# Optimization experiments

Measured on AMD Instinct MI355X. Metric: run time of the kernel, lower is better.

Reference implementation:

```python
import jax, jax.numpy as jnp
import numpy as np

T, N, E = 12, 2048, 32768
X_DIM, H_DIM, Z_DIM, NL = 128, 256, 32, 2
EPS = 1e-10


def setup_inputs() -> dict:
    key = jax.random.key(0)
    ks = jax.random.split(key, 24)
    s = 0.1  # reset_parameters stdv
    p = {}
    p['x'] = jax.random.normal(ks[0], (T, N, X_DIM), jnp.float32)
    p['edge_index'] = jax.random.randint(ks[1], (T, 2, E), 0, N, dtype=jnp.int32)
    p['adj'] = (jax.random.uniform(ks[2], (T, N, N)) < 0.01).astype(jnp.float32)
    p['eps_src'] = jax.random.normal(ks[3], (T, N, Z_DIM), jnp.float32)
    p['eps_dst'] = jax.random.normal(ks[4], (T, N, Z_DIM), jnp.float32)
    p['phi_x_w'] = s * jax.random.normal(ks[5], (X_DIM, H_DIM), jnp.float32)
    p['phi_z_w'] = s * jax.random.normal(ks[6], (2 * Z_DIM, H_DIM), jnp.float32)
    p['gru_xw0'] = s * jax.random.normal(ks[7], (3, 2 * H_DIM, H_DIM), jnp.float32)  # (z,r,h) layer 0
    p['gru_xw1'] = s * jax.random.normal(ks[8], (3, H_DIM, H_DIM), jnp.float32)      # (z,r,h) layer 1
    p['gru_hw'] = s * jax.random.normal(ks[9], (NL, 3, H_DIM, H_DIM), jnp.float32)
    p['enc_w'] = s * jax.random.normal(ks[10], (2, 2 * H_DIM, H_DIM), jnp.float32)   # [src,dst]
    p['enc_b'] = s * jax.random.normal(ks[11], (2, H_DIM), jnp.float32)
    p['mean_w'] = s * jax.random.normal(ks[12], (2, H_DIM, Z_DIM), jnp.float32)
    p['mean_b'] = s * jax.random.normal(ks[13], (2, Z_DIM), jnp.float32)
    p['std_w'] = s * jax.random.normal(ks[14], (2, H_DIM, Z_DIM), jnp.float32)
    p['std_b'] = s * jax.random.normal(ks[15], (2, Z_DIM), jnp.float32)
    p['pri_w'] = s * jax.random.normal(ks[16], (2, H_DIM, H_DIM), jnp.float32)
    p['pri_b'] = s * jax.random.normal(ks[17], (2, H_DIM), jnp.float32)
    p['pri_mw'] = s * jax.random.normal(ks[18], (2, H_DIM, Z_DIM), jnp.float32)
    p['pri_mb'] = s * jax.random.normal(ks[19], (2, Z_DIM), jnp.float32)
    p['pri_sw'] = s * jax.random.normal(ks[20], (2, H_DIM, Z_DIM), jnp.float32)
    p['pri_sb'] = s * jax.random.normal(ks[21], (2, Z_DIM), jnp.float32)
    return p


def _gin_pre(x, src, dst):
    # GIN (eps=0): x + sum_{(src->dst)} x[src]; linear applied by caller
    return x + jax.ops.segment_sum(x[src], dst, num_segments=N)


def _gcn(x, w, b, src, dst):
    # GCNConv with self-loops and symmetric normalization
    deg = jax.ops.segment_sum(jnp.ones(src.shape[0], x.dtype), dst, num_segments=N) + 1.0
    dinv = deg ** -0.5
    nrm = dinv[src] * dinv[dst]
    xw = x @ w
    agg = jax.ops.segment_sum(nrm[:, None] * xw[src], dst, num_segments=N)
    return agg + xw / deg[:, None] + b


def _kld(m1, s1, m2, s2):
    k = (2 * jnp.log(s2 + EPS) - 2 * jnp.log(s1 + EPS)
         + ((s1 + EPS) ** 2 + (m1 - m2) ** 2) / (s2 + EPS) ** 2 - 1.0)
    return 0.5 / N * jnp.mean(jnp.sum(k, axis=1))


def reference(x, edge_index, adj, eps_src, eps_dst, phi_x_w, phi_z_w,
              gru_xw0, gru_xw1, gru_hw, enc_w, enc_b, mean_w, mean_b,
              std_w, std_b, pri_w, pri_b, pri_mw, pri_mb, pri_sw, pri_sb):
    h0 = jnp.zeros((NL, N, H_DIM), x.dtype)

    def step(h, inp):
        x_t, e_t, a_t, es_t, ed_t = inp
        src, dst = e_t[0], e_t[1]
        phi_x_t = jax.nn.relu(x_t @ phi_x_w)
        cat = jnp.concatenate([phi_x_t, h[-1]], axis=1)  # [N, 2H]
        cat_pre = _gin_pre(cat, src, dst)
        enc_s = jax.nn.relu(cat_pre @ enc_w[0] + enc_b[0])
        enc_d = jax.nn.relu(cat_pre @ enc_w[1] + enc_b[1])
        mean_s = _gcn(enc_s, mean_w[0], mean_b[0], src, dst)
        std_s = jax.nn.softplus(_gin_pre(enc_s, src, dst) @ std_w[0] + std_b[0])
        mean_d = _gcn(enc_d, mean_w[1], mean_b[1], src, dst)
        std_d = jax.nn.softplus(_gin_pre(enc_d, src, dst) @ std_w[1] + std_b[1])
        pri_s = jax.nn.relu(h[-1] @ pri_w[0] + pri_b[0])
        pm_s = pri_s @ pri_mw[0] + pri_mb[0]
        ps_s = jax.nn.softplus(pri_s @ pri_sw[0] + pri_sb[0])
        pri_d = jax.nn.relu(h[-1] @ pri_w[1] + pri_b[1])
        pm_d = pri_d @ pri_mw[1] + pri_mb[1]
        ps_d = jax.nn.softplus(pri_d @ pri_sw[1] + pri_sb[1])
        z_s = mean_s + std_s * es_t
        z_d = mean_d + std_d * ed_t
        phi_z_t = jax.nn.relu(jnp.concatenate([z_s, z_d], axis=1) @ phi_z_w)
        dec = z_s @ z_d.T  # [N, N] inner-product decoder (identity act)
        # graph-GRU across layers
        g_in = jnp.concatenate([phi_x_t, phi_z_t], axis=1)  # [N, 2H]
        new_h = []
        for i in range(NL):
            xi = g_in if i == 0 else new_h[i - 1]
            xw = gru_xw0 if i == 0 else gru_xw1
            xpre = _gin_pre(xi, src, dst)
            hpre = _gin_pre(h[i], src, dst)
            z_g = jax.nn.sigmoid(xpre @ xw[0] + hpre @ gru_hw[i, 0])
            r_g = jax.nn.sigmoid(xpre @ xw[1] + hpre @ gru_hw[i, 1])
            h_t = jnp.tanh(xpre @ xw[2] + _gin_pre(r_g * h[i], src, dst) @ gru_hw[i, 2])
            new_h.append(z_g * h[i] + (1.0 - z_g) * h_t)
        h_new = jnp.stack(new_h)
        kld = _kld(mean_s, std_s, pm_s, ps_s) + _kld(mean_d, std_d, pm_d, ps_d)
        ssum = a_t.sum()
        nn2 = jnp.asarray(N * N, a_t.dtype)
        posw = (nn2 - ssum) / ssum
        norm = nn2 / ((nn2 - ssum) * 2.0)
        bce = -posw * a_t * jax.nn.log_sigmoid(dec) - (1.0 - a_t) * jax.nn.log_sigmoid(-dec)
        nll = norm * jnp.mean(bce)
        return h_new, (kld, nll, dec)

    _, (klds, nlls, decs) = jax.lax.scan(step, h0, (x, edge_index, adj, eps_src, eps_dst))
    return jnp.sum(klds), jnp.sum(nlls), decs
```

## Files before the change

### kernel.cpp

```cpp
#include <hip/hip_runtime.h>
#include <math.h>

#define NTS 12
#define NND 2048
#define NED 32768
#define XDI 128
#define HDI 256
#define ZDI 32
#define EPSC 1e-10f
#define NH ((size_t)NND * HDI)
#define NZ ((size_t)NND * ZDI)
#define ZPL ((size_t)NND * 64)
#define XSZ ((size_t)NTS * NND * XDI)

typedef unsigned short u16;
typedef __bf16 bf16x8 __attribute__((ext_vector_type(8)));
typedef float f32x4 __attribute__((ext_vector_type(4)));

#define MF(a, b, c) __builtin_amdgcn_mfma_f32_16x16x32_bf16(a, b, c, 0, 0, 0)


__device__ __forceinline__ float lsigf(float x) {
    return fminf(x, 0.f) - log1pf(expf(-fabsf(x)));
}
__device__ __forceinline__ float splus(float v) {
    return fmaxf(v, 0.f) + log1pf(expf(-fabsf(v)));
}
__device__ __forceinline__ u16 f2b(float f) {
    unsigned u = __float_as_uint(f);
    u += 0x7fffu + ((u >> 16) & 1u);
    return (u16)(u >> 16);
}
__device__ __forceinline__ float b2f(u16 b) {
    return __uint_as_float((unsigned)b << 16);
}
__device__ __forceinline__ void f2b2(float v, u16& hi, u16& lo) {
    hi = f2b(v);
    lo = f2b(v - b2f(hi));
}
__device__ __forceinline__ void st_b16(u16* buf, size_t plane, size_t idx, float v) {
    u16 hi, lo;
    f2b2(v, hi, lo);
    buf[idx] = hi;
    buf[plane + idx] = lo;
}
__device__ __forceinline__ void st_b16v4(u16* buf, size_t plane, size_t idx, float4 v) {
    ushort4 h, l;
    f2b2(v.x, h.x, l.x); f2b2(v.y, h.y, l.y);
    f2b2(v.z, h.z, l.z); f2b2(v.w, h.w, l.w);
    *(ushort4*)(buf + idx) = h;
    *(ushort4*)(buf + plane + idx) = l;
}
__device__ __forceinline__ float4 ld_hl4(const u16* b, size_t plane, size_t idx) {
    ushort4 h = *(const ushort4*)(b + idx);
    ushort4 l = *(const ushort4*)(b + plane + idx);
    float4 r;
    r.x = b2f(h.x) + b2f(l.x); r.y = b2f(h.y) + b2f(l.y);
    r.z = b2f(h.z) + b2f(l.z); r.w = b2f(h.w) + b2f(l.w);
    return r;
}
__device__ float4 gin_hl(const u16* buf, size_t plane, int n, const int* __restrict__ offs,
                         const int* __restrict__ cs, int lane) {
    int e0 = offs[n], e1 = offs[n + 1];
    size_t c4 = (size_t)lane * 4;
    float4 a0 = ld_hl4(buf, plane, (size_t)n * HDI + c4);
    float4 a1 = {0.f, 0.f, 0.f, 0.f}, a2 = {0.f, 0.f, 0.f, 0.f}, a3 = {0.f, 0.f, 0.f, 0.f};
    int j = e0;
    for (; j + 3 < e1; j += 4) {
        int s0 = cs[j], s1 = cs[j + 1], s2 = cs[j + 2], s3 = cs[j + 3];
        float4 v0 = ld_hl4(buf, plane, (size_t)s0 * HDI + c4);
        float4 v1 = ld_hl4(buf, plane, (size_t)s1 * HDI + c4);
        float4 v2 = ld_hl4(buf, plane, (size_t)s2 * HDI + c4);
        float4 v3 = ld_hl4(buf, plane, (size_t)s3 * HDI + c4);
        a0.x += v0.x; a0.y += v0.y; a0.z += v0.z; a0.w += v0.w;
        a1.x += v1.x; a1.y += v1.y; a1.z += v1.z; a1.w += v1.w;
        a2.x += v2.x; a2.y += v2.y; a2.z += v2.z; a2.w += v2.w;
        a3.x += v3.x; a3.y += v3.y; a3.z += v3.z; a3.w += v3.w;
    }
    for (; j < e1; ++j) {
        float4 v = ld_hl4(buf, plane, (size_t)cs[j] * HDI + c4);
        a0.x += v.x; a0.y += v.y; a0.z += v.z; a0.w += v.w;
    }
    a0.x += a1.x + a2.x + a3.x;
    a0.y += a1.y + a2.y + a3.y;
    a0.z += a1.z + a2.z + a3.z;
    a0.w += a1.w + a2.w + a3.w;
    return a0;
}

__host__ __device__ inline size_t wtoff(int m) {
    if (m == 0) return 0;
    if (m == 1) return 65536;
    return 98304 + (size_t)(m - 2) * 131072;
}

__device__ __forceinline__ void mm64(f32x4* A12, const u16* __restrict__ Ahi, size_t apl,
                                     const u16* __restrict__ Bt, int K,
                                     int row0, int cc, int lr, int kg) {
    const u16* bp = Bt + (size_t)(cc * 16 + lr) * K + kg;
    const u16* blp = bp + (size_t)K * HDI;
    const u16* ap0 = Ahi + (size_t)(row0 + lr) * K + kg;
    for (int k0 = 0; k0 < K; k0 += 32) {
        bf16x8 bh = *(const bf16x8*)(bp + k0);
        bf16x8 bl = *(const bf16x8*)(blp + k0);
#pragma unroll
        for (int s = 0; s < 4; s++) {
            const u16* ap = ap0 + (size_t)(16 * s) * K;
            bf16x8 ah = *(const bf16x8*)(ap + k0);
            bf16x8 al = *(const bf16x8*)(ap + apl + k0);
            A12[s * 3 + 0] = MF(ah, bh, A12[s * 3 + 0]);
            A12[s * 3 + 1] = MF(al, bh, A12[s * 3 + 1]);
            A12[s * 3 + 2] = MF(ah, bl, A12[s * 3 + 2]);
        }
    }
}

__device__ __forceinline__ void epi_hl(f32x4* A12, u16* dst, size_t plane,
                                       int row0, int cc, int lane, int relu) {
    int col = cc * 16 + (lane & 15);
    int rb0 = (lane >> 4) << 2;
#pragma unroll
    for (int s = 0; s < 4; s++)
#pragma unroll
        for (int i = 0; i < 4; i++) {
            int row = row0 + s * 16 + rb0 + i;
            float v = A12[s * 3][i] + A12[s * 3 + 1][i] + A12[s * 3 + 2][i];
            if (relu) v = fmaxf(v, 0.f);
            st_b16(dst, plane, (size_t)row * HDI + col, v);
        }
}


__global__ __launch_bounds__(256) void k0_setup(const int* __restrict__ ei,
                                                const float* __restrict__ x,
                                                const float* w_phix, const float* w_phiz,
                                                const float* w_enc, const float* w_pri,
                                                const float* w_gx0, const float* w_gx1,
                                                const float* w_gh,
                                                u16* __restrict__ warena, u16* __restrict__ xb,
                                                int* __restrict__ counts) {
    const int bid = blockIdx.x, tid = threadIdx.x;
    if (bid < 1536) {
        int idx = bid * 256 + tid;
        int t = idx >> 15, e = idx & (NED - 1);
        atomicAdd(&counts[t * NND + ei[(size_t)t * 2 * NED + NED + e]], 1);
    } else if (bid < 7424) {
        int u = bid - 1536;
        int m = u >> 8, k = u & 255;
        const int Kt = (m == 0) ? 128 : (m == 1) ? 64 : 256;
        if (k < Kt) {
            const int srcsel[23] = {0, 1, 2, 2, 2, 2, 3, 3, 4, 4, 4, 4,
                                    4, 4, 6, 6, 6, 5, 5, 5, 6, 6, 6};
            const int srcoff[23] = {0, 0, 0, 65536, 131072, 196608, 0, 65536,
                                    0, 65536, 131072, 196608, 262144, 327680,
                                    0, 65536, 131072, 0, 65536, 131072,
                                    196608, 262144, 327680};
            const float* srcs[7] = {w_phix, w_phiz, w_enc, w_pri, w_gx0, w_gx1, w_gh};
            const float* W = srcs[srcsel[m]] + srcoff[m];
            u16* D = warena + wtoff(m);
            float v = W[(size_t)k * 256 + tid];
            u16 hi, lo;
            f2b2(v, hi, lo);
            D[(size_t)tid * Kt + k] = hi;
            D[(size_t)Kt * 256 + (size_t)tid * Kt + k] = lo;
        }
    } else {
        size_t i = (size_t)(bid - 7424) * 256 + tid;
        float4 v = ((const float4*)x)[i];
        ushort4 h, l;
        f2b2(v.x, h.x, l.x); f2b2(v.y, h.y, l.y);
        f2b2(v.z, h.z, l.z); f2b2(v.w, h.w, l.w);
        ((ushort4*)xb)[i] = h;
        ((ushort4*)(xb + XSZ))[i] = l;
    }
}

__global__ __launch_bounds__(256) void k1_scan_phix(const int* __restrict__ counts,
                                                    int* __restrict__ offs,
                                                    float* __restrict__ deg,
                                                    float* __restrict__ dinv,
                                                    const u16* __restrict__ xb,
                                                    const u16* __restrict__ warena,
                                                    u16* __restrict__ phixb) {
    __shared__ int tsum[256];
    const int bid = blockIdx.x, tid = threadIdx.x;
    if (bid < 12) {
        const int* cnt = counts + bid * NND;
        int* off = offs + bid * (NND + 1);
        float* dg = deg + bid * NND;
        float* dv = dinv + bid * NND;
        int base = tid * 8;
        int local[8];
        int s = 0;
        for (int i = 0; i < 8; i++) { local[i] = s; s += cnt[base + i]; }
        tsum[tid] = s;
        __syncthreads();
        for (int o = 1; o < 256; o <<= 1) {
            int v = (tid >= o) ? tsum[tid - o] : 0;
            __syncthreads();
            tsum[tid] += v;
            __syncthreads();
        }
        int excl = tsum[tid] - s;
        for (int i = 0; i < 8; i++) off[base + i] = excl + local[i];
        if (tid == 255) off[NND] = excl + s;
        for (int i = 0; i < 8; i++) {
            float d = (float)cnt[base + i] + 1.0f;
            dg[base + i] = d;
            dv[base + i] = 1.0f / sqrtf(d);
        }
    } else {
        int u = bid - 12;
        int t = u >> 7, tile = u & 127;
        const int wid = tid >> 6, lane = tid & 63;
        const int lr = lane & 15, kg = (lane >> 4) * 8;
        int row0 = (tile >> 4) * 256 + wid * 64, cc = tile & 15;
        f32x4 A12[12] = {};
        mm64(A12, xb + (size_t)t * NND * XDI, XSZ, warena + wtoff(0), XDI, row0, cc, lr, kg);
        epi_hl(A12, phixb + (size_t)t * 2 * NH, NH, row0, cc, lane, 1);
    }
}

__global__ __launch_bounds__(256) void k2_fill(const int* __restrict__ ei,
                                               const int* __restrict__ offs,
                                               int* __restrict__ cursor,
                                               const float* __restrict__ dinv,
                                               int* __restrict__ csrc,
                                               float* __restrict__ csrw) {
    int idx = blockIdx.x * 256 + threadIdx.x;
    int t = idx >> 15, e = idx & (NED - 1);
    const int* src = ei + (size_t)t * 2 * NED;
    const int* dst = src + NED;
    int d = dst[e], s = src[e];
    const int* off_t = offs + t * (NND + 1);
    int pos = off_t[d] + atomicAdd(&cursor[t * NND + d], 1);
    csrc[(size_t)t * NED + pos] = s;
    csrw[(size_t)t * NED + pos] = dinv[t * NND + s] * dinv[t * NND + d];
}


__global__ __launch_bounds__(256) void kA(const u16* __restrict__ phxt,
                                          const u16* __restrict__ h1b,
                                          const u16* __restrict__ warena,
                                          u16* __restrict__ Ub, float* __restrict__ prif,
                                          const float* __restrict__ b_pri) {
    const int bid = blockIdx.x, tid = threadIdx.x;
    const int wid = tid >> 6, lane = tid & 63;
    const int lr = lane & 15, kg = (lane >> 4) * 8;
    f32x4 A12[12] = {};
    if (bid < 256) {
        int o = bid >> 7, tile = bid & 127;
        int row0 = (tile >> 4) * 256 + wid * 64, cc = tile & 15;
        mm64(A12, phxt, NH, warena + wtoff(2 + 2 * o), HDI, row0, cc, lr, kg);
        mm64(A12, h1b, NH, warena + wtoff(3 + 2 * o), HDI, row0, cc, lr, kg);
        epi_hl(A12, Ub + (size_t)o * 2 * NH, NH, row0, cc, lane, 0);
    } else {
        int q = bid - 256;
        int o = q >> 7, tile = q & 127;
        int row0 = (tile >> 4) * 256 + wid * 64, cc = tile & 15;
        mm64(A12, h1b, NH, warena + wtoff(6 + o), HDI, row0, cc, lr, kg);
        int col = cc * 16 + lr;
        int rb0 = (lane >> 4) << 2;
        float* C = prif + (size_t)o * NH;
        float bv = b_pri[o * HDI + col];
#pragma unroll
        for (int s = 0; s < 4; s++)
#pragma unroll
            for (int i = 0; i < 4; i++) {
                int row = row0 + s * 16 + rb0 + i;
                float v = A12[s * 3][i] + A12[s * 3 + 1][i] + A12[s * 3 + 2][i] + bv;
                C[(size_t)row * HDI + col] = fmaxf(v, 0.f);
            }
    }
}

__global__ __launch_bounds__(256) void kB(const u16* __restrict__ Ub,
                                          const float* __restrict__ prif,
                                          const int* __restrict__ offs,
                                          const int* __restrict__ cs,
                                          const float* __restrict__ b_enc,
                                          const float* __restrict__ w_mean,
                                          const float* __restrict__ w_std,
                                          const float* __restrict__ w_pm,
                                          const float* __restrict__ b_pm,
                                          const float* __restrict__ w_ps,
                                          const float* __restrict__ b_ps,
                                          float* __restrict__ xw, float* __restrict__ pmps) {
    __shared__ float rowbuf[4][256];
    const int tid = threadIdx.x;
    const int wid = tid >> 6, lane = tid & 63;
    const int u = blockIdx.x * 4 + wid;
    if (u < 4096) {
        int seg = u >> 11, n = u & 2047;
        float4 a = gin_hl(Ub + (size_t)seg * 2 * NH, NH, n, offs, cs, lane);
        const float* eb = b_enc + seg * HDI + lane * 4;
        a.x = fmaxf(a.x + eb[0], 0.f);
        a.y = fmaxf(a.y + eb[1], 0.f);
        a.z = fmaxf(a.z + eb[2], 0.f);
        a.w = fmaxf(a.w + eb[3], 0.f);
        *(float4*)&rowbuf[wid][lane * 4] = a;
        const float* B = ((lane < 32) ? w_mean : w_std) + seg * 8192;
        int m = lane & 31;
        float acc = 0.f;
        const float* rb = rowbuf[wid];
#pragma unroll 8
        for (int k = 0; k < 256; k++) acc += rb[k] * B[k * 32 + m];
        float* O = xw + ((lane < 32) ? seg : 2 + seg) * NZ;
        O[(size_t)n * ZDI + m] = acc;
    } else {
        int q = u - 4096;
        int s = q >> 10, unit = q & 1023;
        int n = unit * 2 + (lane >> 5);
        int m = lane & 31;
        const float* A = prif + ((s < 2) ? 0 : NH);
        const float* B = (s & 1) ? (w_ps + (s >> 1) * 8192) : (w_pm + (s >> 1) * 8192);
        const float* bi = (s & 1) ? (b_ps + (s >> 1) * 32) : (b_pm + (s >> 1) * 32);
        float acc = bi[m];
        const float* ar = A + (size_t)n * HDI;
#pragma unroll 4
        for (int k = 0; k < 256; k += 4) {
            float4 a4 = *(const float4*)(ar + k);
            acc += a4.x * B[(k + 0) * 32 + m];
            acc += a4.y * B[(k + 1) * 32 + m];
            acc += a4.z * B[(k + 2) * 32 + m];
            acc += a4.w * B[(k + 3) * 32 + m];
        }
        if (s & 1) acc = splus(acc);
        pmps[(size_t)s * NZ + (size_t)n * ZDI + m] = acc;
    }
}

__global__ __launch_bounds__(256) void kC(const float* __restrict__ xw,
                                          const float* __restrict__ pmps,
                                          const int* __restrict__ offs,
                                          const int* __restrict__ cs,
                                          const float* __restrict__ cw,
                                          const float* __restrict__ dgv,
                                          const float* __restrict__ b_mean,
                                          const float* __restrict__ b_std,
                                          const float* __restrict__ es,
                                          const float* __restrict__ ed,
                                          float* __restrict__ zcatf, u16* __restrict__ zcatb,
                                          double* __restrict__ accd) {
    __shared__ double smd[4];
    const int tid = threadIdx.x;
    const int wid = tid >> 6, lane = tid & 63;
    const int n = blockIdx.x * 4 + wid;
    const int sel = lane >> 5, m = lane & 31;
    const float* xwm = xw + (size_t)sel * NZ;
    const float* xws = xw + (size_t)(2 + sel) * NZ;
    int e0 = offs[n], e1 = offs[n + 1];
    float am0 = 0.f, am1 = 0.f, am2 = 0.f, am3 = 0.f;
    float as0 = xws[(size_t)n * ZDI + m], as1 = 0.f, as2 = 0.f, as3 = 0.f;
    int j = e0;
    for (; j + 3 < e1; j += 4) {
        int s0 = cs[j], s1 = cs[j + 1], s2 = cs[j + 2], s3 = cs[j + 3];
        am0 += cw[j] * xwm[(size_t)s0 * ZDI + m];
        am1 += cw[j + 1] * xwm[(size_t)s1 * ZDI + m];
        am2 += cw[j + 2] * xwm[(size_t)s2 * ZDI + m];
        am3 += cw[j + 3] * xwm[(size_t)s3 * ZDI + m];
        as0 += xws[(size_t)s0 * ZDI + m];
        as1 += xws[(size_t)s1 * ZDI + m];
        as2 += xws[(size_t)s2 * ZDI + m];
        as3 += xws[(size_t)s3 * ZDI + m];
    }
    for (; j < e1; ++j) {
        int s = cs[j];
        am0 += cw[j] * xwm[(size_t)s * ZDI + m];
        as0 += xws[(size_t)s * ZDI + m];
    }
    float am = am0 + am1 + am2 + am3;
    float as_ = as0 + as1 + as2 + as3;
    float mean = am + xwm[(size_t)n * ZDI + m] / dgv[n] + b_mean[sel * 32 + m];
    float sd = splus(as_ + b_std[sel * 32 + m]);
    const float* eps = sel ? ed : es;
    float z = mean + sd * eps[(size_t)n * ZDI + m];
    size_t zi = (size_t)n * 64 + sel * 32 + m;
    zcatf[zi] = z;
    st_b16(zcatb, ZPL, zi, z);
    float pm = pmps[(size_t)(sel * 2) * NZ + (size_t)n * ZDI + m];
    float ps = pmps[(size_t)(sel * 2 + 1) * NZ + (size_t)n * ZDI + m];
    float a1v = sd + EPSC, a2v = ps + EPSC;
    float dm = mean - pm;
    double kl = (double)(2.f * (logf(a2v) - logf(a1v)) +
                         (a1v * a1v + dm * dm) / (a2v * a2v) - 1.f);
#pragma unroll
    for (int o = 32; o > 0; o >>= 1) kl += __shfl_down(kl, o);
    if (lane == 0) smd[wid] = kl;
    __syncthreads();
    if (tid == 0) atomicAdd(accd, smd[0] + smd[1] + smd[2] + smd[3]);
}

__global__ __launch_bounds__(256) void kD(const float* __restrict__ zcatf,
                                          const u16* __restrict__ zcatb,
                                          const float* __restrict__ adjt,
                                          const u16* __restrict__ warena,
                                          float* __restrict__ dect,
                                          u16* __restrict__ phizb,
                                          double* __restrict__ bcet) {
    __shared__ float smf[2 * 32 * 68];
    const int bid = blockIdx.x, tid = threadIdx.x;
    if (bid < 1024) {
        float (*zsS)[68] = (float(*)[68])smf;
        float (*zdS)[68] = (float(*)[68])(smf + 32 * 68);
        const int tx = tid & 15, ty = tid >> 4;
        const int c0 = (bid & 31) * 64, r0 = (bid >> 5) * 64;
        const int lrow = tid >> 2;
        const int lk = (tid & 3) * 8;
        float4 v0 = *(const float4*)&zcatf[(size_t)(r0 + lrow) * 64 + lk];
        float4 v1 = *(const float4*)&zcatf[(size_t)(r0 + lrow) * 64 + lk + 4];
        float4 w0 = *(const float4*)&zcatf[(size_t)(c0 + lrow) * 64 + 32 + lk];
        float4 w1 = *(const float4*)&zcatf[(size_t)(c0 + lrow) * 64 + 32 + lk + 4];
        zsS[lk + 0][lrow] = v0.x; zsS[lk + 1][lrow] = v0.y; zsS[lk + 2][lrow] = v0.z; zsS[lk + 3][lrow] = v0.w;
        zsS[lk + 4][lrow] = v1.x; zsS[lk + 5][lrow] = v1.y; zsS[lk + 6][lrow] = v1.z; zsS[lk + 7][lrow] = v1.w;
        zdS[lk + 0][lrow] = w0.x; zdS[lk + 1][lrow] = w0.y; zdS[lk + 2][lrow] = w0.z; zdS[lk + 3][lrow] = w0.w;
        zdS[lk + 4][lrow] = w1.x; zdS[lk + 5][lrow] = w1.y; zdS[lk + 6][lrow] = w1.z; zdS[lk + 7][lrow] = w1.w;
        __syncthreads();

        float acc[4][4] = {};
#pragma unroll
        for (int k = 0; k < 32; k++) {
            const float4 a4 = *(const float4*)&zsS[k][ty * 4];
            const float4 b4 = *(const float4*)&zdS[k][tx * 4];
            const float aa[4] = {a4.x, a4.y, a4.z, a4.w};
            const float bb[4] = {b4.x, b4.y, b4.z, b4.w};
#pragma unroll
            for (int i = 0; i < 4; i++)
#pragma unroll
                for (int j = 0; j < 4; j++) acc[i][j] += aa[i] * bb[j];
        }

        float pa = 0.f, p1 = 0.f, p2 = 0.f;
#pragma unroll
        for (int i = 0; i < 4; i++) {
            const int r = r0 + ty * 4 + i;
            const float4 av4 = *(const float4*)&adjt[(size_t)r * NND + c0 + tx * 4];
            const float av[4] = {av4.x, av4.y, av4.z, av4.w};
            float* drow = &dect[(size_t)r * NND + c0 + tx * 4];
#pragma unroll
            for (int j = 0; j < 4; j++) {
                float d = acc[i][j];
                __builtin_nontemporal_store(d, &drow[j]);
                float a = av[j];
                pa += a;
                p1 += a * lsigf(d);
                p2 += (1.f - a) * lsigf(-d);
            }
        }
        __syncthreads();
        smf[tid] = pa; smf[256 + tid] = p1; smf[512 + tid] = p2;
        __syncthreads();
        for (int o = 128; o > 0; o >>= 1) {
            if (tid < o) {
                smf[tid] += smf[tid + o];
                smf[256 + tid] += smf[256 + tid + o];
                smf[512 + tid] += smf[512 + tid + o];
            }
            __syncthreads();
        }
        if (tid == 0) {
            double* b = bcet + (size_t)bid * 3;
            b[0] = (double)smf[0];
            b[1] = (double)smf[256];
            b[2] = (double)smf[512];
        }
    } else {
        int u = bid - 1024;
        const int wid = tid >> 6, lane = tid & 63;
        const int lr = lane & 15, kg = (lane >> 4) * 8;
        int row0 = (u >> 4) * 256 + wid * 64, cc = u & 15;
        f32x4 A12[12] = {};
        mm64(A12, zcatb, ZPL, warena + wtoff(1), 64, row0, cc, lr, kg);
        epi_hl(A12, phizb, NH, row0, cc, lane, 1);
    }
}

__global__ __launch_bounds__(256) void kE(const u16* __restrict__ phxt,
                                          const u16* __restrict__ phizb,
                                          const u16* __restrict__ h0b,
                                          const u16* __restrict__ warena,
                                          u16* __restrict__ Pb) {
    const int bid = blockIdx.x, tid = threadIdx.x;
    const int wid = tid >> 6, lane = tid & 63;
    const int lr = lane & 15, kg = (lane >> 4) * 8;
    int o = bid >> 7, tile = bid & 127;
    int row0 = (tile >> 4) * 256 + wid * 64, cc = tile & 15;
    f32x4 A12[12] = {};
    if (o == 0) {
        mm64(A12, phxt, NH, warena + wtoff(8), HDI, row0, cc, lr, kg);
        mm64(A12, phizb, NH, warena + wtoff(9), HDI, row0, cc, lr, kg);
        mm64(A12, h0b, NH, warena + wtoff(14), HDI, row0, cc, lr, kg);
    } else if (o == 1) {
        mm64(A12, phxt, NH, warena + wtoff(10), HDI, row0, cc, lr, kg);
        mm64(A12, phizb, NH, warena + wtoff(11), HDI, row0, cc, lr, kg);
        mm64(A12, h0b, NH, warena + wtoff(15), HDI, row0, cc, lr, kg);
    } else {
        mm64(A12, phxt, NH, warena + wtoff(12), HDI, row0, cc, lr, kg);
        mm64(A12, phizb, NH, warena + wtoff(13), HDI, row0, cc, lr, kg);
    }
    epi_hl(A12, Pb + (size_t)o * 2 * NH, NH, row0, cc, lane, 0);
}

__global__ __launch_bounds__(256) void kE1(const u16* __restrict__ nh0b,
                                           const u16* __restrict__ h1b,
                                           const u16* __restrict__ warena,
                                           u16* __restrict__ Pb) {
    const int bid = blockIdx.x, tid = threadIdx.x;
    const int wid = tid >> 6, lane = tid & 63;
    const int lr = lane & 15, kg = (lane >> 4) * 8;
    int o = bid >> 7, tile = bid & 127;
    int row0 = (tile >> 4) * 256 + wid * 64, cc = tile & 15;
    f32x4 A12[12] = {};
    if (o == 0) {
        mm64(A12, nh0b, NH, warena + wtoff(17), HDI, row0, cc, lr, kg);
        mm64(A12, h1b, NH, warena + wtoff(20), HDI, row0, cc, lr, kg);
    } else if (o == 1) {
        mm64(A12, nh0b, NH, warena + wtoff(18), HDI, row0, cc, lr, kg);
        mm64(A12, h1b, NH, warena + wtoff(21), HDI, row0, cc, lr, kg);
    } else {
        mm64(A12, nh0b, NH, warena + wtoff(19), HDI, row0, cc, lr, kg);
    }
    epi_hl(A12, Pb + (size_t)o * 2 * NH, NH, row0, cc, lane, 0);
}

__global__ __launch_bounds__(256) void kF(const u16* __restrict__ Pb,
                                          const u16* __restrict__ hb,
                                          float* __restrict__ zGf, u16* __restrict__ rhb,
                                          const int* __restrict__ offs,
                                          const int* __restrict__ cs) {
    const int tid = threadIdx.x;
    const int wid = tid >> 6, lane = tid & 63;
    const int u = blockIdx.x * 4 + wid;
    int seg = u >> 11, n = u & 2047;
    size_t idx = (size_t)n * HDI + lane * 4;
    if (seg == 0) {
        float4 a = gin_hl(Pb, NH, n, offs, cs, lane);
        a.x = 1.f / (1.f + expf(-a.x)); a.y = 1.f / (1.f + expf(-a.y));
        a.z = 1.f / (1.f + expf(-a.z)); a.w = 1.f / (1.f + expf(-a.w));
        *(float4*)&zGf[idx] = a;
    } else {
        float4 a = gin_hl(Pb + 2 * NH, NH, n, offs, cs, lane);
        float4 h4 = ld_hl4(hb, NH, idx);
        float4 rh;
        rh.x = h4.x / (1.f + expf(-a.x)); rh.y = h4.y / (1.f + expf(-a.y));
        rh.z = h4.z / (1.f + expf(-a.z)); rh.w = h4.w / (1.f + expf(-a.w));
        st_b16v4(rhb, NH, idx, rh);
    }
}

__global__ __launch_bounds__(256) void kG(const u16* __restrict__ rhb,
                                          const u16* __restrict__ warena, int wtm,
                                          const u16* __restrict__ Pb, u16* __restrict__ Rb) {
    const int bid = blockIdx.x, tid = threadIdx.x;
    const int wid = tid >> 6, lane = tid & 63;
    const int lr = lane & 15, kg = (lane >> 4) * 8;
    int row0 = (bid >> 4) * 256 + wid * 64, cc = bid & 15;
    f32x4 A12[12] = {};
    mm64(A12, rhb, NH, warena + wtoff(wtm), HDI, row0, cc, lr, kg);
    const u16* Ph = Pb + 4 * NH;
    int col = cc * 16 + lr;
    int rb0 = (lane >> 4) << 2;
#pragma unroll
    for (int s = 0; s < 4; s++)
#pragma unroll
        for (int i = 0; i < 4; i++) {
            int row = row0 + s * 16 + rb0 + i;
            size_t idx = (size_t)row * HDI + col;
            float v = A12[s * 3][i] + A12[s * 3 + 1][i] + A12[s * 3 + 2][i] +
                      b2f(Ph[idx]) + b2f(Ph[NH + idx]);
            st_b16(Rb, NH, idx, v);
        }
}

__global__ __launch_bounds__(256) void kH(const u16* __restrict__ Rb,
                                          const float* __restrict__ zGf,
                                          const u16* __restrict__ hb,
                                          u16* __restrict__ nhb,
                                          const int* __restrict__ offs,
                                          const int* __restrict__ cs) {
    const int tid = threadIdx.x;
    const int wid = tid >> 6, lane = tid & 63;
    const int n = blockIdx.x * 4 + wid;
    size_t idx = (size_t)n * HDI + lane * 4;
    float4 a = gin_hl(Rb, NH, n, offs, cs, lane);
    float4 z4 = *(const float4*)&zGf[idx];
    float4 h4 = ld_hl4(hb, NH, idx);
    float4 o;
    o.x = z4.x * h4.x + (1.f - z4.x) * tanhf(a.x);
    o.y = z4.y * h4.y + (1.f - z4.y) * tanhf(a.y);
    o.z = z4.z * h4.z + (1.f - z4.z) * tanhf(a.z);
    o.w = z4.w * h4.w + (1.f - z4.w) * tanhf(a.w);
    st_b16v4(nhb, NH, idx, o);
}

__global__ __launch_bounds__(256) void kFin(const double* __restrict__ accd,
                                            const double* __restrict__ bce,
                                            float* __restrict__ out) {
    __shared__ double sums[36];
    const int tid = threadIdx.x;
    const int wid = tid >> 6, lane = tid & 63;
    for (int p = wid; p < 36; p += 4) {
        int t = p / 3, c = p % 3;
        double s = 0.0;
        for (int i = lane; i < 1024; i += 64) s += bce[((size_t)t * 1024 + i) * 3 + c];
#pragma unroll
        for (int o = 32; o > 0; o >>= 1) s += __shfl_down(s, o);
        if (lane == 0) sums[p] = s;
    }
    __syncthreads();
    if (tid == 0) {
        const double nn2 = (double)NND * (double)NND;
        out[0] = (float)(0.5 * accd[0] / nn2);
        double nll = 0.0;
        for (int t = 0; t < NTS; ++t) {
            double s = sums[t * 3 + 0];
            double S1 = sums[t * 3 + 1];
            double S2 = sums[t * 3 + 2];
            double posw = (nn2 - s) / s;
            double norm = nn2 / ((nn2 - s) * 2.0);
            nll += norm * (-posw * S1 - S2) / nn2;
        }
        out[1] = (float)nll;
    }
}


extern "C" void kernel_launch(void* const* d_in, const int* in_sizes, int n_in,
                              void* d_out, int out_size, void* d_ws, size_t ws_size,
                              hipStream_t stream) {
    (void)in_sizes; (void)n_in; (void)out_size; (void)ws_size;

    const float* x_all = (const float*)d_in[0];
    const int* ei_all = (const int*)d_in[1];
    const float* adj_all = (const float*)d_in[2];
    const float* eps_s_all = (const float*)d_in[3];
    const float* eps_d_all = (const float*)d_in[4];
    const float* phi_x_w = (const float*)d_in[5];
    const float* phi_z_w = (const float*)d_in[6];
    const float* gru_xw0 = (const float*)d_in[7];
    const float* gru_xw1 = (const float*)d_in[8];
    const float* gru_hw = (const float*)d_in[9];
    const float* enc_w = (const float*)d_in[10];
    const float* enc_b = (const float*)d_in[11];
    const float* mean_w = (const float*)d_in[12];
    const float* mean_b = (const float*)d_in[13];
    const float* std_w = (const float*)d_in[14];
    const float* std_b = (const float*)d_in[15];
    const float* pri_w = (const float*)d_in[16];
    const float* pri_b = (const float*)d_in[17];
    const float* pri_mw = (const float*)d_in[18];
    const float* pri_mb = (const float*)d_in[19];
    const float* pri_sw = (const float*)d_in[20];
    const float* pri_sb = (const float*)d_in[21];
    float* out = (float*)d_out;

    size_t off = 0;
    auto alloc = [&](size_t bytes) -> void* {
        void* p = (char*)d_ws + off;
        off = (off + bytes + 255) & ~(size_t)255;
        return p;
    };

    u16* warena = (u16*)alloc(2850816 * 2);
    u16* xb = (u16*)alloc(2 * XSZ * 2);
    u16* phixb = (u16*)alloc((size_t)NTS * 2 * NH * 2);
    u16* hbuf = (u16*)alloc(8 * NH * 2);
    u16* Ub = (u16*)alloc(4 * NH * 2);
    float* prif = (float*)alloc(2 * NH * 4);
    float* xw = (float*)alloc(4 * NZ * 4);
    float* pmps = (float*)alloc(4 * NZ * 4);
    float* zcatf = (float*)alloc(ZPL * 4);
    u16* zcatb = (u16*)alloc(2 * ZPL * 2);
    u16* phizb = (u16*)alloc(2 * NH * 2);
    u16* Pb = (u16*)alloc(6 * NH * 2);
    float* zGf = (float*)alloc(NH * 4);
    u16* rhb = (u16*)alloc(2 * NH * 2);
    u16* Rb = (u16*)alloc(2 * NH * 2);
    float* deg = (float*)alloc((size_t)NTS * NND * 4);
    float* dinv = (float*)alloc((size_t)NTS * NND * 4);
    int* counts = (int*)alloc(2 * (size_t)NTS * NND * 4);
    int* cursor = counts + (size_t)NTS * NND;
    int* offs = (int*)alloc((size_t)NTS * (NND + 1) * 4);
    int* csrc = (int*)alloc((size_t)NTS * NED * 4);
    float* csrw = (float*)alloc((size_t)NTS * NED * 4);
    double* accd = (double*)alloc(8 * 8);
    double* bce = (double*)alloc((size_t)NTS * 1024 * 3 * 8);

    u16* h0b[2] = {hbuf, hbuf + 2 * NH};
    u16* h1b[2] = {hbuf + 4 * NH, hbuf + 6 * NH};

    hipMemsetAsync(hbuf, 0, 8 * NH * 2, stream);
    hipMemsetAsync(counts, 0, 2 * (size_t)NTS * NND * 4, stream);
    hipMemsetAsync(accd, 0, 8 * 8, stream);

    k0_setup<<<10496, 256, 0, stream>>>(ei_all, x_all, phi_x_w, phi_z_w, enc_w, pri_w,
                                        gru_xw0, gru_xw1, gru_hw, warena, xb, counts);
    k1_scan_phix<<<12 + 1536, 256, 0, stream>>>(counts, offs, deg, dinv, xb, warena, phixb);
    k2_fill<<<1536, 256, 0, stream>>>(ei_all, offs, cursor, dinv, csrc, csrw);

    for (int t = 0; t < NTS; ++t) {
        const int cur = t & 1;
        const int* off_t = offs + (size_t)t * (NND + 1);
        const int* cs_t = csrc + (size_t)t * NED;
        const float* cw_t = csrw + (size_t)t * NED;
        const float* dg_t = deg + (size_t)t * NND;
        const u16* phxt = phixb + (size_t)t * 2 * NH;
        const float* adj_t = adj_all + (size_t)t * NND * NND;
        float* dec_t = out + 2 + (size_t)t * NND * NND;
        const float* es_t = eps_s_all + (size_t)t * NZ;
        const float* ed_t = eps_d_all + (size_t)t * NZ;
        double* bce_t = bce + (size_t)t * 1024 * 3;

        kA<<<512, 256, 0, stream>>>(phxt, h1b[cur], warena, Ub, prif, pri_b);
        kB<<<2048, 256, 0, stream>>>(Ub, prif, off_t, cs_t, enc_b, mean_w, std_w,
                                     pri_mw, pri_mb, pri_sw, pri_sb, xw, pmps);
        kC<<<512, 256, 0, stream>>>(xw, pmps, off_t, cs_t, cw_t, dg_t, mean_b, std_b,
                                    es_t, ed_t, zcatf, zcatb, accd);
        kD<<<1152, 256, 0, stream>>>(zcatf, zcatb, adj_t, warena, dec_t, phizb, bce_t);
        kE<<<384, 256, 0, stream>>>(phxt, phizb, h0b[cur], warena, Pb);
        kF<<<1024, 256, 0, stream>>>(Pb, h0b[cur], zGf, rhb, off_t, cs_t);
        kG<<<128, 256, 0, stream>>>(rhb, warena, 16, Pb, Rb);
        kH<<<512, 256, 0, stream>>>(Rb, zGf, h0b[cur], h0b[cur ^ 1], off_t, cs_t);
        kE1<<<384, 256, 0, stream>>>(h0b[cur ^ 1], h1b[cur], warena, Pb);
        kF<<<1024, 256, 0, stream>>>(Pb, h1b[cur], zGf, rhb, off_t, cs_t);
        kG<<<128, 256, 0, stream>>>(rhb, warena, 22, Pb, Rb);
        kH<<<512, 256, 0, stream>>>(Rb, zGf, h1b[cur], h1b[cur ^ 1], off_t, cs_t);
    }

    kFin<<<1, 256, 0, stream>>>(accd, bce, out);
}
```

Measured before the change: 3.033 ms.

## Spread decoder tiles across GRU kernels and fuse phi_z, GIN gate, and matmul

The standalone decoder kernel is removed. Its 1024 tiles are spread as extra blocks over the six GRU kernels so the memory-bound decoder work runs alongside the GRU matmul and gather work. The phi_z projection moves into kC as a per-row FP32 dot product. kF and kG are fused into kFG, which keeps r*h in LDS as split hi/lo bf16 and runs the MFMA from there, so the rhb round-trip through global memory disappears. In exchange, kernels get extra LDS and divergent block roles, and the decoder adjacency read is spread unevenly.

```diff
diff --git a/kernel.cpp b/kernel.cpp
--- a/kernel.cpp
+++ b/kernel.cpp
@@ -12,6 +12,9 @@
 #define NZ ((size_t)NND * ZDI)
 #define ZPL ((size_t)NND * 64)
 #define XSZ ((size_t)NTS * NND * XDI)
+#define LSTR 264
+#define LPH (16 * 264)
+#define DECF 171
 
 typedef unsigned short u16;
 typedef __bf16 bf16x8 __attribute__((ext_vector_type(8)));
@@ -114,6 +117,23 @@
         }
     }
 }
+__device__ __forceinline__ void mml16(f32x4* a12, const u16* lds,
+                                      const u16* __restrict__ Bt, int K,
+                                      int ctbase, int lr, int kg) {
+    for (int k0 = 0; k0 < K; k0 += 32) {
+        bf16x8 ah = *(const bf16x8*)(lds + lr * LSTR + kg + k0);
+        bf16x8 al = *(const bf16x8*)(lds + LPH + lr * LSTR + kg + k0);
+#pragma unroll
+        for (int ct = 0; ct < 4; ct++) {
+            const u16* bp = Bt + (size_t)((ctbase + ct) * 16 + lr) * K + kg + k0;
+            bf16x8 bh = *(const bf16x8*)bp;
+            bf16x8 bl = *(const bf16x8*)(bp + (size_t)K * HDI);
+            a12[ct * 3 + 0] = MF(ah, bh, a12[ct * 3 + 0]);
+            a12[ct * 3 + 1] = MF(al, bh, a12[ct * 3 + 1]);
+            a12[ct * 3 + 2] = MF(ah, bl, a12[ct * 3 + 2]);
+        }
+    }
+}
 
 __device__ __forceinline__ void epi_hl(f32x4* A12, u16* dst, size_t plane,
                                        int row0, int cc, int lane, int relu) {
@@ -128,6 +148,74 @@
             if (relu) v = fmaxf(v, 0.f);
             st_b16(dst, plane, (size_t)row * HDI + col, v);
         }
+}
+
+__device__ void dec_tile(const float* __restrict__ zcatf, const float* __restrict__ adjt,
+                         float* __restrict__ dect, double* __restrict__ bcet,
+                         int db, int tid, float* smf) {
+    float (*zsS)[68] = (float(*)[68])smf;
+    float (*zdS)[68] = (float(*)[68])(smf + 32 * 68);
+    const int tx = tid & 15, ty = tid >> 4;
+    const int c0 = (db & 31) * 64, r0 = (db >> 5) * 64;
+    const int lrow = tid >> 2;
+    const int lk = (tid & 3) * 8;
+    float4 v0 = *(const float4*)&zcatf[(size_t)(r0 + lrow) * 64 + lk];
+    float4 v1 = *(const float4*)&zcatf[(size_t)(r0 + lrow) * 64 + lk + 4];
+    float4 w0 = *(const float4*)&zcatf[(size_t)(c0 + lrow) * 64 + 32 + lk];
+    float4 w1 = *(const float4*)&zcatf[(size_t)(c0 + lrow) * 64 + 32 + lk + 4];
+    zsS[lk + 0][lrow] = v0.x; zsS[lk + 1][lrow] = v0.y; zsS[lk + 2][lrow] = v0.z; zsS[lk + 3][lrow] = v0.w;
+    zsS[lk + 4][lrow] = v1.x; zsS[lk + 5][lrow] = v1.y; zsS[lk + 6][lrow] = v1.z; zsS[lk + 7][lrow] = v1.w;
+    zdS[lk + 0][lrow] = w0.x; zdS[lk + 1][lrow] = w0.y; zdS[lk + 2][lrow] = w0.z; zdS[lk + 3][lrow] = w0.w;
+    zdS[lk + 4][lrow] = w1.x; zdS[lk + 5][lrow] = w1.y; zdS[lk + 6][lrow] = w1.z; zdS[lk + 7][lrow] = w1.w;
+    __syncthreads();
+
+    float acc[4][4] = {};
+#pragma unroll
+    for (int k = 0; k < 32; k++) {
+        const float4 a4 = *(const float4*)&zsS[k][ty * 4];
+        const float4 b4 = *(const float4*)&zdS[k][tx * 4];
+        const float aa[4] = {a4.x, a4.y, a4.z, a4.w};
+        const float bb[4] = {b4.x, b4.y, b4.z, b4.w};
+#pragma unroll
+        for (int i = 0; i < 4; i++)
+#pragma unroll
+            for (int j = 0; j < 4; j++) acc[i][j] += aa[i] * bb[j];
+    }
+
+    float pa = 0.f, p1 = 0.f, p2 = 0.f;
+#pragma unroll
+    for (int i = 0; i < 4; i++) {
+        const int r = r0 + ty * 4 + i;
+        const float4 av4 = *(const float4*)&adjt[(size_t)r * NND + c0 + tx * 4];
+        const float av[4] = {av4.x, av4.y, av4.z, av4.w};
+        float* drow = &dect[(size_t)r * NND + c0 + tx * 4];
+#pragma unroll
+        for (int j = 0; j < 4; j++) {
+            float d = acc[i][j];
+            __builtin_nontemporal_store(d, &drow[j]);
+            float a = av[j];
+            pa += a;
+            p1 += a * lsigf(d);
+            p2 += (1.f - a) * lsigf(-d);
+        }
+    }
+    __syncthreads();
+    smf[tid] = pa; smf[256 + tid] = p1; smf[512 + tid] = p2;
+    __syncthreads();
+    for (int o = 128; o > 0; o >>= 1) {
+        if (tid < o) {
+            smf[tid] += smf[tid + o];
+            smf[256 + tid] += smf[256 + tid + o];
+            smf[512 + tid] += smf[512 + tid + o];
+        }
+        __syncthreads();
+    }
+    if (tid == 0) {
+        double* b = bcet + (size_t)db * 3;
+        b[0] = (double)smf[0];
+        b[1] = (double)smf[256];
+        b[2] = (double)smf[512];
+    }
 }
 
 
@@ -340,8 +428,11 @@
                                           const float* __restrict__ b_std,
                                           const float* __restrict__ es,
                                           const float* __restrict__ ed,
-                                          float* __restrict__ zcatf, u16* __restrict__ zcatb,
+                                          const float* __restrict__ w_phiz,
+                                          float* __restrict__ zcatf,
+                                          u16* __restrict__ phizb,
                                           double* __restrict__ accd) {
+    __shared__ float zrow[4][64];
     __shared__ double smd[4];
     const int tid = threadIdx.x;
     const int wid = tid >> 6, lane = tid & 63;
@@ -377,13 +468,28 @@
     float z = mean + sd * eps[(size_t)n * ZDI + m];
     size_t zi = (size_t)n * 64 + sel * 32 + m;
     zcatf[zi] = z;
-    st_b16(zcatb, ZPL, zi, z);
+    zrow[wid][sel * 32 + m] = z;
     float pm = pmps[(size_t)(sel * 2) * NZ + (size_t)n * ZDI + m];
     float ps = pmps[(size_t)(sel * 2 + 1) * NZ + (size_t)n * ZDI + m];
     float a1v = sd + EPSC, a2v = ps + EPSC;
     float dm = mean - pm;
     double kl = (double)(2.f * (logf(a2v) - logf(a1v)) +
                          (a1v * a1v + dm * dm) / (a2v * a2v) - 1.f);
+    {
+        const float* zr = zrow[wid];
+        const int cbase = lane * 4;
+        float a0 = 0.f, a1 = 0.f, a2 = 0.f, a3 = 0.f;
+#pragma unroll 4
+        for (int k = 0; k < 64; k++) {
+            float zv = zr[k];
+            const float* wr = w_phiz + k * 256 + cbase;
+            a0 += zv * wr[0]; a1 += zv * wr[1]; a2 += zv * wr[2]; a3 += zv * wr[3];
+        }
+        float4 r;
+        r.x = fmaxf(a0, 0.f); r.y = fmaxf(a1, 0.f);
+        r.z = fmaxf(a2, 0.f); r.w = fmaxf(a3, 0.f);
+        st_b16v4(phizb, NH, (size_t)n * HDI + cbase, r);
+    }
 #pragma unroll
     for (int o = 32; o > 0; o >>= 1) kl += __shfl_down(kl, o);
     if (lane == 0) smd[wid] = kl;
@@ -391,96 +497,22 @@
     if (tid == 0) atomicAdd(accd, smd[0] + smd[1] + smd[2] + smd[3]);
 }
 
-__global__ __launch_bounds__(256) void kD(const float* __restrict__ zcatf,
-                                          const u16* __restrict__ zcatb,
-                                          const float* __restrict__ adjt,
-                                          const u16* __restrict__ warena,
-                                          float* __restrict__ dect,
-                                          u16* __restrict__ phizb,
-                                          double* __restrict__ bcet) {
-    __shared__ float smf[2 * 32 * 68];
-    const int bid = blockIdx.x, tid = threadIdx.x;
-    if (bid < 1024) {
-        float (*zsS)[68] = (float(*)[68])smf;
-        float (*zdS)[68] = (float(*)[68])(smf + 32 * 68);
-        const int tx = tid & 15, ty = tid >> 4;
-        const int c0 = (bid & 31) * 64, r0 = (bid >> 5) * 64;
-        const int lrow = tid >> 2;
-        const int lk = (tid & 3) * 8;
-        float4 v0 = *(const float4*)&zcatf[(size_t)(r0 + lrow) * 64 + lk];
-        float4 v1 = *(const float4*)&zcatf[(size_t)(r0 + lrow) * 64 + lk + 4];
-        float4 w0 = *(const float4*)&zcatf[(size_t)(c0 + lrow) * 64 + 32 + lk];
-        float4 w1 = *(const float4*)&zcatf[(size_t)(c0 + lrow) * 64 + 32 + lk + 4];
-        zsS[lk + 0][lrow] = v0.x; zsS[lk + 1][lrow] = v0.y; zsS[lk + 2][lrow] = v0.z; zsS[lk + 3][lrow] = v0.w;
-        zsS[lk + 4][lrow] = v1.x; zsS[lk + 5][lrow] = v1.y; zsS[lk + 6][lrow] = v1.z; zsS[lk + 7][lrow] = v1.w;
-        zdS[lk + 0][lrow] = w0.x; zdS[lk + 1][lrow] = w0.y; zdS[lk + 2][lrow] = w0.z; zdS[lk + 3][lrow] = w0.w;
-        zdS[lk + 4][lrow] = w1.x; zdS[lk + 5][lrow] = w1.y; zdS[lk + 6][lrow] = w1.z; zdS[lk + 7][lrow] = w1.w;
-        __syncthreads();
-
-        float acc[4][4] = {};
-#pragma unroll
-        for (int k = 0; k < 32; k++) {
-            const float4 a4 = *(const float4*)&zsS[k][ty * 4];
-            const float4 b4 = *(const float4*)&zdS[k][tx * 4];
-            const float aa[4] = {a4.x, a4.y, a4.z, a4.w};
-            const float bb[4] = {b4.x, b4.y, b4.z, b4.w};
-#pragma unroll
-            for (int i = 0; i < 4; i++)
-#pragma unroll
-                for (int j = 0; j < 4; j++) acc[i][j] += aa[i] * bb[j];
-        }
-
-        float pa = 0.f, p1 = 0.f, p2 = 0.f;
-#pragma unroll
-        for (int i = 0; i < 4; i++) {
-            const int r = r0 + ty * 4 + i;
-            const float4 av4 = *(const float4*)&adjt[(size_t)r * NND + c0 + tx * 4];
-            const float av[4] = {av4.x, av4.y, av4.z, av4.w};
-            float* drow = &dect[(size_t)r * NND + c0 + tx * 4];
-#pragma unroll
-            for (int j = 0; j < 4; j++) {
-                float d = acc[i][j];
-                __builtin_nontemporal_store(d, &drow[j]);
-                float a = av[j];
-                pa += a;
-                p1 += a * lsigf(d);
-                p2 += (1.f - a) * lsigf(-d);
-            }
-        }
-        __syncthreads();
-        smf[tid] = pa; smf[256 + tid] = p1; smf[512 + tid] = p2;
-        __syncthreads();
-        for (int o = 128; o > 0; o >>= 1) {
-            if (tid < o) {
-                smf[tid] += smf[tid + o];
-                smf[256 + tid] += smf[256 + tid + o];
-                smf[512 + tid] += smf[512 + tid + o];
-            }
-            __syncthreads();
-        }
-        if (tid == 0) {
-            double* b = bcet + (size_t)bid * 3;
-            b[0] = (double)smf[0];
-            b[1] = (double)smf[256];
-            b[2] = (double)smf[512];
-        }
-    } else {
-        int u = bid - 1024;
-        const int wid = tid >> 6, lane = tid & 63;
-        const int lr = lane & 15, kg = (lane >> 4) * 8;
-        int row0 = (u >> 4) * 256 + wid * 64, cc = u & 15;
-        f32x4 A12[12] = {};
-        mm64(A12, zcatb, ZPL, warena + wtoff(1), 64, row0, cc, lr, kg);
-        epi_hl(A12, phizb, NH, row0, cc, lane, 1);
-    }
-}
-
 __global__ __launch_bounds__(256) void kE(const u16* __restrict__ phxt,
                                           const u16* __restrict__ phizb,
                                           const u16* __restrict__ h0b,
                                           const u16* __restrict__ warena,
-                                          u16* __restrict__ Pb) {
+                                          u16* __restrict__ Pb,
+                                          const float* __restrict__ zcatf,
+                                          const float* __restrict__ adjt,
+                                          float* __restrict__ dect,
+                                          double* __restrict__ bcet,
+                                          int nmain, int decbase) {
+    __shared__ __align__(16) float smf[2 * 32 * 68];
     const int bid = blockIdx.x, tid = threadIdx.x;
+    if (bid >= nmain) {
+        dec_tile(zcatf, adjt, dect, bcet, decbase + bid - nmain, tid, smf);
+        return;
+    }
     const int wid = tid >> 6, lane = tid & 63;
     const int lr = lane & 15, kg = (lane >> 4) * 8;
     int o = bid >> 7, tile = bid & 127;
@@ -504,8 +536,18 @@
 __global__ __launch_bounds__(256) void kE1(const u16* __restrict__ nh0b,
                                            const u16* __restrict__ h1b,
                                            const u16* __restrict__ warena,
-                                           u16* __restrict__ Pb) {
+                                           u16* __restrict__ Pb,
+                                           const float* __restrict__ zcatf,
+                                           const float* __restrict__ adjt,
+                                           float* __restrict__ dect,
+                                           double* __restrict__ bcet,
+                                           int nmain, int decbase) {
+    __shared__ __align__(16) float smf[2 * 32 * 68];
     const int bid = blockIdx.x, tid = threadIdx.x;
+    if (bid >= nmain) {
+        dec_tile(zcatf, adjt, dect, bcet, decbase + bid - nmain, tid, smf);
+        return;
+    }
     const int wid = tid >> 6, lane = tid & 63;
     const int lr = lane & 15, kg = (lane >> 4) * 8;
     int o = bid >> 7, tile = bid & 127;
@@ -523,50 +565,60 @@
     epi_hl(A12, Pb + (size_t)o * 2 * NH, NH, row0, cc, lane, 0);
 }
 
-__global__ __launch_bounds__(256) void kF(const u16* __restrict__ Pb,
-                                          const u16* __restrict__ hb,
-                                          float* __restrict__ zGf, u16* __restrict__ rhb,
-                                          const int* __restrict__ offs,
-                                          const int* __restrict__ cs) {
-    const int tid = threadIdx.x;
+__global__ __launch_bounds__(256) void kFG(const u16* __restrict__ Pb,
+                                           const u16* __restrict__ hb,
+                                           const u16* __restrict__ warena, int wtm,
+                                           float* __restrict__ zGf, u16* __restrict__ Rb,
+                                           const int* __restrict__ offs,
+                                           const int* __restrict__ cs,
+                                           const float* __restrict__ zcatf,
+                                           const float* __restrict__ adjt,
+                                           float* __restrict__ dect,
+                                           double* __restrict__ bcet,
+                                           int nmain, int decbase) {
+    __shared__ __align__(16) char smem[17408];
+    const int bid = blockIdx.x, tid = threadIdx.x;
+    if (bid >= nmain) {
+        dec_tile(zcatf, adjt, dect, bcet, decbase + bid - nmain, tid, (float*)smem);
+        return;
+    }
+    u16* lrh = (u16*)smem;
     const int wid = tid >> 6, lane = tid & 63;
-    const int u = blockIdx.x * 4 + wid;
-    int seg = u >> 11, n = u & 2047;
-    size_t idx = (size_t)n * HDI + lane * 4;
-    if (seg == 0) {
-        float4 a = gin_hl(Pb, NH, n, offs, cs, lane);
-        a.x = 1.f / (1.f + expf(-a.x)); a.y = 1.f / (1.f + expf(-a.y));
-        a.z = 1.f / (1.f + expf(-a.z)); a.w = 1.f / (1.f + expf(-a.w));
-        *(float4*)&zGf[idx] = a;
-    } else {
-        float4 a = gin_hl(Pb + 2 * NH, NH, n, offs, cs, lane);
+    const int lr = lane & 15, kg = (lane >> 4) * 8;
+    const int n0 = bid * 16;
+    const int c4 = lane * 4;
+    for (int rr = 0; rr < 4; rr++) {
+        int rl = wid * 4 + rr, n = n0 + rl;
+        size_t idx = (size_t)n * HDI + c4;
+        float4 az = gin_hl(Pb, NH, n, offs, cs, lane);
+        float4 zg;
+        zg.x = 1.f / (1.f + expf(-az.x)); zg.y = 1.f / (1.f + expf(-az.y));
+        zg.z = 1.f / (1.f + expf(-az.z)); zg.w = 1.f / (1.f + expf(-az.w));
+        *(float4*)&zGf[idx] = zg;
+        float4 ar = gin_hl(Pb + 2 * NH, NH, n, offs, cs, lane);
         float4 h4 = ld_hl4(hb, NH, idx);
         float4 rh;
-        rh.x = h4.x / (1.f + expf(-a.x)); rh.y = h4.y / (1.f + expf(-a.y));
-        rh.z = h4.z / (1.f + expf(-a.z)); rh.w = h4.w / (1.f + expf(-a.w));
-        st_b16v4(rhb, NH, idx, rh);
-    }
-}
-
-__global__ __launch_bounds__(256) void kG(const u16* __restrict__ rhb,
-                                          const u16* __restrict__ warena, int wtm,
-                                          const u16* __restrict__ Pb, u16* __restrict__ Rb) {
-    const int bid = blockIdx.x, tid = threadIdx.x;
-    const int wid = tid >> 6, lane = tid & 63;
-    const int lr = lane & 15, kg = (lane >> 4) * 8;
-    int row0 = (bid >> 4) * 256 + wid * 64, cc = bid & 15;
-    f32x4 A12[12] = {};
-    mm64(A12, rhb, NH, warena + wtoff(wtm), HDI, row0, cc, lr, kg);
+        rh.x = h4.x / (1.f + expf(-ar.x)); rh.y = h4.y / (1.f + expf(-ar.y));
+        rh.z = h4.z / (1.f + expf(-ar.z)); rh.w = h4.w / (1.f + expf(-ar.w));
+        ushort4 hh, ll;
+        f2b2(rh.x, hh.x, ll.x); f2b2(rh.y, hh.y, ll.y);
+        f2b2(rh.z, hh.z, ll.z); f2b2(rh.w, hh.w, ll.w);
+        *(ushort4*)(lrh + rl * LSTR + c4) = hh;
+        *(ushort4*)(lrh + LPH + rl * LSTR + c4) = ll;
+    }
+    __syncthreads();
+    f32x4 a12[12] = {};
+    mml16(a12, lrh, warena + wtoff(wtm), 256, wid * 4, lr, kg);
     const u16* Ph = Pb + 4 * NH;
-    int col = cc * 16 + lr;
-    int rb0 = (lane >> 4) << 2;
-#pragma unroll
-    for (int s = 0; s < 4; s++)
+    int rb0 = (lane >> 4) * 4;
+#pragma unroll
+    for (int ct = 0; ct < 4; ct++)
 #pragma unroll
         for (int i = 0; i < 4; i++) {
-            int row = row0 + s * 16 + rb0 + i;
+            int row = n0 + rb0 + i;
+            int col = (wid * 4 + ct) * 16 + lr;
             size_t idx = (size_t)row * HDI + col;
-            float v = A12[s * 3][i] + A12[s * 3 + 1][i] + A12[s * 3 + 2][i] +
+            float v = a12[ct * 3][i] + a12[ct * 3 + 1][i] + a12[ct * 3 + 2][i] +
                       b2f(Ph[idx]) + b2f(Ph[NH + idx]);
             st_b16(Rb, NH, idx, v);
         }
@@ -577,10 +629,21 @@
                                           const u16* __restrict__ hb,
                                           u16* __restrict__ nhb,
                                           const int* __restrict__ offs,
-                                          const int* __restrict__ cs) {
-    const int tid = threadIdx.x;
+                                          const int* __restrict__ cs,
+                                          const float* __restrict__ zcatf,
+                                          const float* __restrict__ adjt,
+                                          float* __restrict__ dect,
+                                          double* __restrict__ bcet,
+                                          int nmain, int decbase, int deccnt) {
+    __shared__ __align__(16) float smf[2 * 32 * 68];
+    const int bid = blockIdx.x, tid = threadIdx.x;
+    if (bid >= nmain) {
+        int db = decbase + bid - nmain;
+        if (db < 1024) dec_tile(zcatf, adjt, dect, bcet, db, tid, smf);
+        return;
+    }
     const int wid = tid >> 6, lane = tid & 63;
-    const int n = blockIdx.x * 4 + wid;
+    const int n = bid * 4 + wid;
     size_t idx = (size_t)n * HDI + lane * 4;
     float4 a = gin_hl(Rb, NH, n, offs, cs, lane);
     float4 z4 = *(const float4*)&zGf[idx];
@@ -670,11 +733,9 @@
     float* xw = (float*)alloc(4 * NZ * 4);
     float* pmps = (float*)alloc(4 * NZ * 4);
     float* zcatf = (float*)alloc(ZPL * 4);
-    u16* zcatb = (u16*)alloc(2 * ZPL * 2);
     u16* phizb = (u16*)alloc(2 * NH * 2);
     u16* Pb = (u16*)alloc(6 * NH * 2);
     float* zGf = (float*)alloc(NH * 4);
-    u16* rhb = (u16*)alloc(2 * NH * 2);
     u16* Rb = (u16*)alloc(2 * NH * 2);
     float* deg = (float*)alloc((size_t)NTS * NND * 4);
     float* dinv = (float*)alloc((size_t)NTS * NND * 4);
@@ -715,16 +776,21 @@
         kB<<<2048, 256, 0, stream>>>(Ub, prif, off_t, cs_t, enc_b, mean_w, std_w,
                                      pri_mw, pri_mb, pri_sw, pri_sb, xw, pmps);
         kC<<<512, 256, 0, stream>>>(xw, pmps, off_t, cs_t, cw_t, dg_t, mean_b, std_b,
-                                    es_t, ed_t, zcatf, zcatb, accd);
-        kD<<<1152, 256, 0, stream>>>(zcatf, zcatb, adj_t, warena, dec_t, phizb, bce_t);
-        kE<<<384, 256, 0, stream>>>(phxt, phizb, h0b[cur], warena, Pb);
-        kF<<<1024, 256, 0, stream>>>(Pb, h0b[cur], zGf, rhb, off_t, cs_t);
-        kG<<<128, 256, 0, stream>>>(rhb, warena, 16, Pb, Rb);
-        kH<<<512, 256, 0, stream>>>(Rb, zGf, h0b[cur], h0b[cur ^ 1], off_t, cs_t);
-        kE1<<<384, 256, 0, stream>>>(h0b[cur ^ 1], h1b[cur], warena, Pb);
-        kF<<<1024, 256, 0, stream>>>(Pb, h1b[cur], zGf, rhb, off_t, cs_t);
-        kG<<<128, 256, 0, stream>>>(rhb, warena, 22, Pb, Rb);
-        kH<<<512, 256, 0, stream>>>(Rb, zGf, h1b[cur], h1b[cur ^ 1], off_t, cs_t);
+                                    es_t, ed_t, phi_z_w, zcatf, phizb, accd);
+        kE<<<384 + DECF, 256, 0, stream>>>(phxt, phizb, h0b[cur], warena, Pb,
+                                           zcatf, adj_t, dec_t, bce_t, 384, 0);
+        kFG<<<128 + DECF, 256, 0, stream>>>(Pb, h0b[cur], warena, 16, zGf, Rb, off_t,
+                                            cs_t, zcatf, adj_t, dec_t, bce_t, 128, DECF);
+        kH<<<512 + DECF, 256, 0, stream>>>(Rb, zGf, h0b[cur], h0b[cur ^ 1], off_t, cs_t,
+                                           zcatf, adj_t, dec_t, bce_t, 512, 2 * DECF, DECF);
+        kE1<<<384 + DECF, 256, 0, stream>>>(h0b[cur ^ 1], h1b[cur], warena, Pb,
+                                            zcatf, adj_t, dec_t, bce_t, 384, 3 * DECF);
+        kFG<<<128 + DECF, 256, 0, stream>>>(Pb, h1b[cur], warena, 22, zGf, Rb, off_t,
+                                            cs_t, zcatf, adj_t, dec_t, bce_t, 128, 4 * DECF);
+        kH<<<512 + (1024 - 5 * DECF), 256, 0, stream>>>(Rb, zGf, h1b[cur], h1b[cur ^ 1],
+                                                        off_t, cs_t, zcatf, adj_t, dec_t,
+                                                        bce_t, 512, 5 * DECF,
+                                                        1024 - 5 * DECF);
     }
 
     kFin<<<1, 256, 0, stream>>>(accd, bce, out);
```

Result: slower. 3.401 ms (+12.1%).
